# Kernel optimization log

Hardware: AMD Instinct MI355X
Metric: run time of the kernel (lower is better)

## Reference

```python
import jax, jax.numpy as jnp
import numpy as np

MAX_SPAN = 16
EPS = 1e-12


def setup_inputs() -> dict:
    key = jax.random.key(0)
    ks = jax.random.split(key, 10)
    B, S, H, R = 64, 512, 768, 51
    embed = jax.random.normal(ks[0], (B, S, H), dtype=jnp.float32)
    sub_head = jax.random.randint(ks[1], (B,), 0, S - MAX_SPAN, dtype=jnp.int32)
    span = jax.random.randint(ks[2], (B,), 0, MAX_SPAN, dtype=jnp.int32)
    sub_tail = sub_head + span  # guaranteed valid span inside [0, S)
    s = 0.02
    W_ih = jax.random.normal(ks[3], (4 * H, H), dtype=jnp.float32) * s
    W_hh = jax.random.normal(ks[4], (4 * H, H), dtype=jnp.float32) * s
    b_ih = jnp.zeros((4 * H,), dtype=jnp.float32)
    b_hh = jnp.zeros((4 * H,), dtype=jnp.float32)
    cln_weight = jnp.ones((H,), dtype=jnp.float32)
    cln_bias = jnp.zeros((H,), dtype=jnp.float32)
    # nonzero so the conditional path is exercised (init is zeros in torch)
    cln_Ww = jax.random.normal(ks[5], (H, H), dtype=jnp.float32) * s
    cln_Wb = jax.random.normal(ks[6], (H, H), dtype=jnp.float32) * s
    Wh = jax.random.normal(ks[7], (R, H), dtype=jnp.float32) * s
    bh = jnp.zeros((R,), dtype=jnp.float32)
    Wt = jax.random.normal(ks[8], (R, H), dtype=jnp.float32) * s
    bt = jnp.zeros((R,), dtype=jnp.float32)
    return {"embed": embed, "sub_head": sub_head, "sub_tail": sub_tail,
            "W_ih": W_ih, "W_hh": W_hh, "b_ih": b_ih, "b_hh": b_hh,
            "cln_weight": cln_weight, "cln_bias": cln_bias,
            "cln_Ww": cln_Ww, "cln_Wb": cln_Wb,
            "Wh": Wh, "bh": bh, "Wt": Wt, "bt": bt}


def _ragged_lstm(embed, sub_head, sub_tail, W_ih, W_hh, b_ih, b_hh):
    # Pack ragged spans [head, tail] into a padded [B, MAX_SPAN, H] block and
    # run one batched LSTM scan, freezing state once past each span's end.
    B, S, H = embed.shape
    offs = jnp.arange(MAX_SPAN, dtype=sub_head.dtype)
    pos = sub_head[:, None] + offs[None, :]                    # [B, T]
    idx = jnp.clip(pos, 0, S - 1)
    x = jnp.take_along_axis(embed, idx[:, :, None], axis=1)    # [B, T, H]
    mask = pos <= sub_tail[:, None]                            # [B, T]

    def step(carry, inp):
        h, c = carry
        xt, mt = inp                                           # [B,H], [B]
        gates = xt @ W_ih.T + b_ih + h @ W_hh.T + b_hh         # [B, 4H]
        i, f, g, o = jnp.split(gates, 4, axis=-1)
        c_new = jax.nn.sigmoid(f) * c + jax.nn.sigmoid(i) * jnp.tanh(g)
        h_new = jax.nn.sigmoid(o) * jnp.tanh(c_new)
        m = mt[:, None]
        h = jnp.where(m, h_new, h)
        c = jnp.where(m, c_new, c)
        return (h, c), None

    h0 = jnp.zeros((B, H), dtype=embed.dtype)
    (hn, _), _ = jax.lax.scan(step, (h0, h0),
                              (x.transpose(1, 0, 2), mask.T))
    return hn                                                  # [B, H]


def _cond_layernorm(inputs, cond, weight, bias, Ww, Wb):
    # weight/bias are conditioned on `cond` via zero-init dense layers
    w = cond @ Ww.T + weight                                   # [B, H]
    b = cond @ Wb.T + bias
    mu = jnp.mean(inputs, axis=-1, keepdims=True)
    xc = inputs - mu
    var = jnp.mean(xc * xc, axis=-1, keepdims=True)
    std = jnp.sqrt(var + EPS)
    return w[:, None, :] * xc / (std + EPS) + b[:, None, :]


def reference(embed, sub_head, sub_tail, W_ih, W_hh, b_ih, b_hh,
              cln_weight, cln_bias, cln_Ww, cln_Wb, Wh, bh, Wt, bt):
    sub_embed = _ragged_lstm(embed, sub_head, sub_tail, W_ih, W_hh, b_ih, b_hh)
    new_embed = _cond_layernorm(embed, sub_embed, cln_weight, cln_bias,
                                cln_Ww, cln_Wb)
    heads = jax.nn.sigmoid(new_embed @ Wh.T + bh)              # [B, S, R]
    tails = jax.nn.sigmoid(new_embed @ Wt.T + bt)
    return heads, tails
```

## Files before the change

### kernel.cpp

```cpp
#include <hip/hip_runtime.h>

typedef __attribute__((ext_vector_type(8))) short bhalf8;
typedef __attribute__((ext_vector_type(4))) float floatx4;

__device__ unsigned short g_whh[3072*768];
__device__ unsigned short g_wih[3072*768];
__device__ unsigned short g_wcln[1536*768];
__device__ unsigned short g_whl[128*768];
__device__ unsigned short g_h2[2*64*768];
__device__ float g_cbuf[64*768];
__device__ float g_xg[16*64*3072];
__device__ float g_wv[64*768], g_bv[64*768];
__device__ float g_bias[3072];
__device__ float g_cw[768], g_cb[768];
__device__ float g_bh[64], g_bt[64];

static __device__ __forceinline__ unsigned short f2bf(float f){
  unsigned u = __builtin_bit_cast(unsigned, f);
  u = (u + 0x7FFFu + ((u >> 16) & 1u)) >> 16;
  return (unsigned short)u;
}
static __device__ __forceinline__ float sigm(float x){ return 1.0f/(1.0f + __expf(-x)); }
static __device__ __forceinline__ float tanhq(float x){ float e = __expf(-2.0f*x); return (1.0f - e)/(1.0f + e); }

static __device__ __forceinline__ void cv8(const float* __restrict__ s, unsigned short* __restrict__ d){
  float4 a = ((const float4*)s)[0];
  float4 b = ((const float4*)s)[1];
  uint4 v;
  v.x = (unsigned)f2bf(a.x) | ((unsigned)f2bf(a.y) << 16);
  v.y = (unsigned)f2bf(a.z) | ((unsigned)f2bf(a.w) << 16);
  v.z = (unsigned)f2bf(b.x) | ((unsigned)f2bf(b.y) << 16);
  v.w = (unsigned)f2bf(b.z) | ((unsigned)f2bf(b.w) << 16);
  *(uint4*)d = v;
}

__global__ __launch_bounds__(256) void casrel_prep(
    const float* __restrict__ W_ih, const float* __restrict__ W_hh,
    const float* __restrict__ Ww,   const float* __restrict__ Wb,
    const float* __restrict__ Wh,   const float* __restrict__ Wt,
    const float* __restrict__ b_ih, const float* __restrict__ b_hh,
    const float* __restrict__ cw,   const float* __restrict__ cb,
    const float* __restrict__ bh,   const float* __restrict__ bt){
  const long CW = 294912;
  const long CC = 147456;
  const long CL = 12288;
  const long CH = 12288;
  const long CF = 6144;
  const long CB = 384, CV = 96, CR = 8;
  const long total = CW*2 + CC + CL + CH + CF + CB + CV*2 + CR*2;
  for(long i = (long)blockIdx.x*256 + threadIdx.x; i < total; i += (long)gridDim.x*256){
    long j = i;
    if(j < CW){ cv8(W_hh + j*8, g_whh + j*8); continue; } j -= CW;
    if(j < CW){ cv8(W_ih + j*8, g_wih + j*8); continue; } j -= CW;
    if(j < CC){ long e = j*8;
                if(e < 589824) cv8(Ww + e, g_wcln + e);
                else           cv8(Wb + (e - 589824), g_wcln + e);
                continue; } j -= CC;
    if(j < CL){ long e = j*8;
                long r = e / 768, k = e - r*768;
                if(r < 51)       cv8(Wh + r*768 + k, g_whl + e);
                else if(r < 102) cv8(Wt + (r-51)*768 + k, g_whl + e);
                else             *(uint4*)(g_whl + e) = make_uint4(0,0,0,0);
                continue; } j -= CL;
    if(j < CH){ *(uint4*)(g_h2 + j*8) = make_uint4(0,0,0,0); continue; } j -= CH;
    if(j < CF){ long e = j*8;
                *(float4*)(g_cbuf + e)     = make_float4(0,0,0,0);
                *(float4*)(g_cbuf + e + 4) = make_float4(0,0,0,0);
                continue; } j -= CF;
    if(j < CB){ long e = j*8;
                #pragma unroll
                for(int q=0;q<8;q++) g_bias[e+q] = b_ih[e+q] + b_hh[e+q];
                continue; } j -= CB;
    if(j < CV){ long e = j*8;
                *(float4*)(g_cw + e)     = *(const float4*)(cw + e);
                *(float4*)(g_cw + e + 4) = *(const float4*)(cw + e + 4);
                continue; } j -= CV;
    if(j < CV){ long e = j*8;
                *(float4*)(g_cb + e)     = *(const float4*)(cb + e);
                *(float4*)(g_cb + e + 4) = *(const float4*)(cb + e + 4);
                continue; } j -= CV;
    if(j < CR){ long e = j*8;
                #pragma unroll
                for(int q=0;q<8;q++){ long n = e+q; g_bh[n] = (n < 51) ? bh[n] : 0.0f; }
                continue; } j -= CR;
    { long e = j*8;
      #pragma unroll
      for(int q=0;q<8;q++){ long n = e+q; g_bt[n] = (n < 51) ? bt[n] : 0.0f; } }
  }
}

__global__ __launch_bounds__(256) void casrel_xgates(
    const float* __restrict__ embed, const int* __restrict__ head){
  __shared__ char sB[128*128];
  const int tid = threadIdx.x, l = tid & 63, w = tid >> 6;
  const int n0 = blockIdx.x * 128;
  const int m0 = blockIdx.y * 64 + w*16;
  const int mrow = m0 + (l & 15);
  const int b = mrow >> 4, t = mrow & 15;
  int pos = head[b] + t; pos = pos < 0 ? 0 : (pos > 511 ? 511 : pos);
  const float* aptr = embed + ((long)b*512 + pos)*768 + ((l >> 4)*8);
  floatx4 acc[8];
  #pragma unroll
  for(int q=0;q<8;q++){ acc[q][0]=0.f; acc[q][1]=0.f; acc[q][2]=0.f; acc[q][3]=0.f; }
  for(int kt=0; kt<12; ++kt){
    __syncthreads();
    #pragma unroll
    for(int j=0;j<4;j++){
      int f = tid + 256*j;
      int row = f >> 3, seg = f & 7;
      uint4 v = *(const uint4*)(g_wih + ((long)(n0+row))*768 + kt*64 + seg*8);
      *(uint4*)(sB + row*128 + ((seg*16) ^ ((row & 7) << 4))) = v;
    }
    __syncthreads();
    #pragma unroll
    for(int ks=0; ks<2; ++ks){
      const int k = kt*64 + ks*32;
      float4 lo = *(const float4*)(aptr + k);
      float4 hi = *(const float4*)(aptr + k + 4);
      bhalf8 a;
      a[0]=(short)f2bf(lo.x); a[1]=(short)f2bf(lo.y); a[2]=(short)f2bf(lo.z); a[3]=(short)f2bf(lo.w);
      a[4]=(short)f2bf(hi.x); a[5]=(short)f2bf(hi.y); a[6]=(short)f2bf(hi.z); a[7]=(short)f2bf(hi.w);
      const int kb = ks*64 + ((l >> 4)*16);
      #pragma unroll
      for(int q=0;q<8;q++){
        int row = q*16 + (l & 15);
        bhalf8 bb = *(const bhalf8*)(sB + row*128 + (kb ^ ((row & 7) << 4)));
        acc[q] = __builtin_amdgcn_mfma_f32_16x16x32_bf16(a, bb, acc[q], 0, 0, 0);
      }
    }
  }
  #pragma unroll
  for(int q=0;q<8;q++){
    const int n = n0 + q*16 + (l & 15);
    const float bias = g_bias[n];
    #pragma unroll
    for(int r=0;r<4;r++){
      const int m = m0 + (l >> 4)*4 + r;
      const int bb2 = m >> 4, tt = m & 15;
      g_xg[((long)(tt*64 + bb2))*3072 + n] = acc[q][r] + bias;
    }
  }
}

__global__ __launch_bounds__(256) void casrel_step(
    const int* __restrict__ head, const int* __restrict__ tail, int t){
  __shared__ char sW[32*1536];
  const unsigned short* hin = g_h2 + (t & 1)*49152;
  unsigned short* hout = g_h2 + ((t & 1) ^ 1)*49152;
  const int tid = threadIdx.x, l = tid & 63, w = tid >> 6;
  const int j0 = blockIdx.x * 8;
  #pragma unroll
  for(int j=0;j<12;j++){
    int f = tid + 256*j;
    int row = f / 96, seg = f - row*96;
    int grow = (row >> 3)*768 + j0 + (row & 7);
    uint4 v = *(const uint4*)(g_whh + (long)grow*768 + seg*8);
    *(uint4*)(sW + row*1536 + ((seg*16) ^ ((row & 7) << 4))) = v;
  }
  __syncthreads();
  const int arow = w*16 + (l & 15);
  floatx4 acc[2];
  #pragma unroll
  for(int q=0;q<2;q++){ acc[q][0]=0.f; acc[q][1]=0.f; acc[q][2]=0.f; acc[q][3]=0.f; }
  const unsigned short* ap = hin + arow*768 + ((l >> 4)*8);
  #pragma unroll 6
  for(int ks=0; ks<24; ++ks){
    bhalf8 a = *(const bhalf8*)(ap + ks*32);
    const int kb = ks*64 + ((l >> 4)*16);
    #pragma unroll
    for(int q=0;q<2;q++){
      int row = q*16 + (l & 15);
      bhalf8 bb = *(const bhalf8*)(sW + row*1536 + (kb ^ ((row & 7) << 4)));
      acc[q] = __builtin_amdgcn_mfma_f32_16x16x32_bf16(a, bb, acc[q], 0, 0, 0);
    }
  }
  const int c = l & 7;
  const int jown = j0 + c;
  const bool lo = (l & 8) == 0;
  #pragma unroll
  for(int r=0;r<4;r++){
    const int b = w*16 + (l >> 4)*4 + r;
    float v0 = acc[0][r], v1 = acc[1][r];
    float o0 = __shfl_xor(v0, 8);
    float o1 = __shfl_xor(v1, 8);
    if(lo){
      const int cell = b*768 + jown;
      const float* xp = g_xg + ((long)(t*64 + b))*3072 + jown;
      float Gi = v0 + xp[0];
      float Gf = o0 + xp[768];
      float Gg = v1 + xp[1536];
      float Go = o1 + xp[2304];
      if(t <= tail[b] - head[b]){
        float cc = g_cbuf[cell];
        float ig = sigm(Gi), fg = sigm(Gf), gg = tanhq(Gg), og = sigm(Go);
        cc = fg*cc + ig*gg;
        g_cbuf[cell] = cc;
        hout[cell] = f2bf(og*tanhq(cc));
      } else {
        hout[cell] = hin[cell];
      }
    }
  }
}

__global__ __launch_bounds__(256) void casrel_clnproj(){
  __shared__ char sW[32*1536];
  const int tid = threadIdx.x, l = tid & 63, w = tid >> 6;
  const int n0c = blockIdx.x * 32;
  #pragma unroll
  for(int j=0;j<12;j++){
    int f = tid + 256*j;
    int row = f / 96, seg = f - row*96;
    uint4 v = *(const uint4*)(g_wcln + (long)(n0c+row)*768 + seg*8);
    *(uint4*)(sW + row*1536 + ((seg*16) ^ ((row & 7) << 4))) = v;
  }
  __syncthreads();
  const int arow = w*16 + (l & 15);
  floatx4 acc2[2];
  #pragma unroll
  for(int q=0;q<2;q++){ acc2[q][0]=0.f; acc2[q][1]=0.f; acc2[q][2]=0.f; acc2[q][3]=0.f; }
  const unsigned short* ap2 = g_h2 + arow*768 + ((l >> 4)*8);
  for(int ks=0; ks<24; ++ks){
    bhalf8 a = *(const bhalf8*)(ap2 + ks*32);
    const int kb = ks*64 + ((l >> 4)*16);
    #pragma unroll
    for(int q=0;q<2;q++){
      int row = q*16 + (l & 15);
      bhalf8 bb = *(const bhalf8*)(sW + row*1536 + (kb ^ ((row & 7) << 4)));
      acc2[q] = __builtin_amdgcn_mfma_f32_16x16x32_bf16(a, bb, acc2[q], 0, 0, 0);
    }
  }
  #pragma unroll
  for(int q=0;q<2;q++){
    const int n = n0c + q*16 + (l & 15);
    #pragma unroll
    for(int r=0;r<4;r++){
      const int b = w*16 + (l >> 4)*4 + r;
      float v = acc2[q][r];
      if(n < 768) g_wv[b*768 + n] = v + g_cw[n];
      else        g_bv[b*768 + (n - 768)] = v + g_cb[n - 768];
    }
  }
}

__global__ __launch_bounds__(256) void casrel_out(
    const float* __restrict__ embed, float* __restrict__ out){
  __shared__ char sB[128*128];
  __shared__ char sE[32*128];
  __shared__ float sMu[32], sRs[32];
  const int tid = threadIdx.x, l = tid & 63, w = tid >> 6;
  const int b = blockIdx.y;
  const int s0 = blockIdx.x * 32;
  const float* xbase = embed + ((long)b*512 + s0)*768;
  for(int rr=0; rr<8; ++rr){
    const int row = w*8 + rr;
    const float* rp = xbase + row*768;
    float sm = 0.f, sq = 0.f;
    #pragma unroll
    for(int q=0;q<3;q++){
      float4 v = *(const float4*)(rp + l*4 + q*256);
      sm += v.x + v.y + v.z + v.w;
      sq += v.x*v.x + v.y*v.y + v.z*v.z + v.w*v.w;
    }
    #pragma unroll
    for(int o=32;o>0;o>>=1){ sm += __shfl_xor(sm, o); sq += __shfl_xor(sq, o); }
    if(l == 0){
      float mu = sm * (1.0f/768.0f);
      float var = sq * (1.0f/768.0f) - mu*mu;
      sMu[row] = mu;
      sRs[row] = 1.0f/(sqrtf(var + 1e-12f) + 1e-12f);
    }
  }
  __syncthreads();
  const int mf = w >> 1, nb = (w & 1)*4;
  floatx4 acc[4];
  #pragma unroll
  for(int q=0;q<4;q++){ acc[q][0]=0.f; acc[q][1]=0.f; acc[q][2]=0.f; acc[q][3]=0.f; }
  for(int kt=0; kt<12; ++kt){
    __syncthreads();
    #pragma unroll
    for(int j=0;j<4;j++){
      int f = tid + 256*j;
      int row = f >> 3, seg = f & 7;
      uint4 v = *(const uint4*)(g_whl + (long)row*768 + kt*64 + seg*8);
      *(uint4*)(sB + row*128 + ((seg*16) ^ ((row & 7) << 4))) = v;
    }
    #pragma unroll
    for(int j=0;j<2;j++){
      int f = tid + 256*j;
      int row = f >> 4, cs = f & 15;
      int k = kt*64 + cs*4;
      float4 x4 = *(const float4*)(xbase + row*768 + k);
      float4 w4 = *(const float4*)(g_wv + b*768 + k);
      float4 c4 = *(const float4*)(g_bv + b*768 + k);
      float mu = sMu[row], rs = sRs[row];
      unsigned long long pk =
          (unsigned long long)f2bf((x4.x - mu)*rs*w4.x + c4.x)
        | ((unsigned long long)f2bf((x4.y - mu)*rs*w4.y + c4.y) << 16)
        | ((unsigned long long)f2bf((x4.z - mu)*rs*w4.z + c4.z) << 32)
        | ((unsigned long long)f2bf((x4.w - mu)*rs*w4.w + c4.w) << 48);
      *(unsigned long long*)(sE + row*128 + ((cs*8) ^ ((row & 7) << 4))) = pk;
    }
    __syncthreads();
    #pragma unroll
    for(int ks=0; ks<2; ++ks){
      const int arow = mf*16 + (l & 15);
      const int kb = ks*64 + ((l >> 4)*16);
      bhalf8 a = *(const bhalf8*)(sE + arow*128 + (kb ^ ((arow & 7) << 4)));
      #pragma unroll
      for(int q=0;q<4;q++){
        int row = (nb + q)*16 + (l & 15);
        bhalf8 bb = *(const bhalf8*)(sB + row*128 + (kb ^ ((row & 7) << 4)));
        acc[q] = __builtin_amdgcn_mfma_f32_16x16x32_bf16(a, bb, acc[q], 0, 0, 0);
      }
    }
  }
  const long HT = (long)64*512*51;
  #pragma unroll
  for(int q=0;q<4;q++){
    const int n = (nb + q)*16 + (l & 15);
    if(n >= 102) continue;
    const int rr = (n < 51) ? n : (n - 51);
    const long obase = (n < 51) ? 0 : HT;
    const float bias = (n < 51) ? g_bh[n] : g_bt[n - 51];
    #pragma unroll
    for(int r=0;r<4;r++){
      const int s = s0 + mf*16 + (l >> 4)*4 + r;
      out[obase + ((long)b*512 + s)*51 + rr] = sigm(acc[q][r] + bias);
    }
  }
}

extern "C" void kernel_launch(void* const* d_in, const int* in_sizes, int n_in,
                              void* d_out, int out_size, void* d_ws, size_t ws_size,
                              hipStream_t stream){
  const float* embed = (const float*)d_in[0];
  const int*   head  = (const int*)d_in[1];
  const int*   tail  = (const int*)d_in[2];
  const float* W_ih  = (const float*)d_in[3];
  const float* W_hh  = (const float*)d_in[4];
  const float* b_ih  = (const float*)d_in[5];
  const float* b_hh  = (const float*)d_in[6];
  const float* cw    = (const float*)d_in[7];
  const float* cb    = (const float*)d_in[8];
  const float* Ww    = (const float*)d_in[9];
  const float* Wb    = (const float*)d_in[10];
  const float* Wh    = (const float*)d_in[11];
  const float* bh    = (const float*)d_in[12];
  const float* Wt    = (const float*)d_in[13];
  const float* bt    = (const float*)d_in[14];
  float* out = (float*)d_out;
  (void)d_ws; (void)ws_size;

  casrel_prep<<<dim3(2048), dim3(256), 0, stream>>>(W_ih, W_hh, Ww, Wb, Wh, Wt,
                                                    b_ih, b_hh, cw, cb, bh, bt);
  casrel_xgates<<<dim3(24,16), dim3(256), 0, stream>>>(embed, head);
  for(int t=0; t<16; ++t)
    casrel_step<<<dim3(96), dim3(256), 0, stream>>>(head, tail, t);
  casrel_clnproj<<<dim3(48), dim3(256), 0, stream>>>();
  casrel_out<<<dim3(16,64), dim3(256), 0, stream>>>(embed, out);
}
```

Before: 245.3 us.

## Convert weights to bf16 on the fly in consumers and store gate preactivations as bf16

Stops pre-converting W_ih and the CLN weights in the prep kernel. The xgates and clnproj kernels now read the fp32 weights and pack them to bf16 while loading tiles. The x-gate buffer is stored as bf16 instead of fp32, halving its write and read traffic. The output kernel double-buffers the normalized-activation tile and reads the projection weights straight from global memory instead of staging them in shared memory. This removes a full weight conversion pass and some barriers, at the cost of extra rounding of the gate preactivations and uncached global B loads.

Result: slower. 276.9 us (+12.9%).

```diff
diff --git a/kernel.cpp b/kernel.cpp
--- a/kernel.cpp
+++ b/kernel.cpp
@@ -4,12 +4,10 @@
 typedef __attribute__((ext_vector_type(4))) float floatx4;
 
 __device__ unsigned short g_whh[3072*768];
-__device__ unsigned short g_wih[3072*768];
-__device__ unsigned short g_wcln[1536*768];
 __device__ unsigned short g_whl[128*768];
 __device__ unsigned short g_h2[2*64*768];
 __device__ float g_cbuf[64*768];
-__device__ float g_xg[16*64*3072];
+__device__ unsigned short g_xg[16*64*3072];
 __device__ float g_wv[64*768], g_bv[64*768];
 __device__ float g_bias[3072];
 __device__ float g_cw[768], g_cb[768];
@@ -20,10 +18,14 @@
   u = (u + 0x7FFFu + ((u >> 16) & 1u)) >> 16;
   return (unsigned short)u;
 }
+static __device__ __forceinline__ float bf2f(unsigned short v){
+  unsigned u = ((unsigned)v) << 16;
+  return __builtin_bit_cast(float, u);
+}
 static __device__ __forceinline__ float sigm(float x){ return 1.0f/(1.0f + __expf(-x)); }
 static __device__ __forceinline__ float tanhq(float x){ float e = __expf(-2.0f*x); return (1.0f - e)/(1.0f + e); }
 
-static __device__ __forceinline__ void cv8(const float* __restrict__ s, unsigned short* __restrict__ d){
+static __device__ __forceinline__ uint4 pk8(const float* __restrict__ s){
   float4 a = ((const float4*)s)[0];
   float4 b = ((const float4*)s)[1];
   uint4 v;
@@ -31,35 +33,28 @@
   v.y = (unsigned)f2bf(a.z) | ((unsigned)f2bf(a.w) << 16);
   v.z = (unsigned)f2bf(b.x) | ((unsigned)f2bf(b.y) << 16);
   v.w = (unsigned)f2bf(b.z) | ((unsigned)f2bf(b.w) << 16);
-  *(uint4*)d = v;
+  return v;
 }
 
 __global__ __launch_bounds__(256) void casrel_prep(
-    const float* __restrict__ W_ih, const float* __restrict__ W_hh,
-    const float* __restrict__ Ww,   const float* __restrict__ Wb,
+    const float* __restrict__ W_hh,
     const float* __restrict__ Wh,   const float* __restrict__ Wt,
     const float* __restrict__ b_ih, const float* __restrict__ b_hh,
     const float* __restrict__ cw,   const float* __restrict__ cb,
     const float* __restrict__ bh,   const float* __restrict__ bt){
   const long CW = 294912;
-  const long CC = 147456;
   const long CL = 12288;
   const long CH = 12288;
   const long CF = 6144;
   const long CB = 384, CV = 96, CR = 8;
-  const long total = CW*2 + CC + CL + CH + CF + CB + CV*2 + CR*2;
+  const long total = CW + CL + CH + CF + CB + CV*2 + CR*2;
   for(long i = (long)blockIdx.x*256 + threadIdx.x; i < total; i += (long)gridDim.x*256){
     long j = i;
-    if(j < CW){ cv8(W_hh + j*8, g_whh + j*8); continue; } j -= CW;
-    if(j < CW){ cv8(W_ih + j*8, g_wih + j*8); continue; } j -= CW;
-    if(j < CC){ long e = j*8;
-                if(e < 589824) cv8(Ww + e, g_wcln + e);
-                else           cv8(Wb + (e - 589824), g_wcln + e);
-                continue; } j -= CC;
+    if(j < CW){ *(uint4*)(g_whh + j*8) = pk8(W_hh + j*8); continue; } j -= CW;
     if(j < CL){ long e = j*8;
                 long r = e / 768, k = e - r*768;
-                if(r < 51)       cv8(Wh + r*768 + k, g_whl + e);
-                else if(r < 102) cv8(Wt + (r-51)*768 + k, g_whl + e);
+                if(r < 51)       *(uint4*)(g_whl + e) = pk8(Wh + r*768 + k);
+                else if(r < 102) *(uint4*)(g_whl + e) = pk8(Wt + (r-51)*768 + k);
                 else             *(uint4*)(g_whl + e) = make_uint4(0,0,0,0);
                 continue; } j -= CL;
     if(j < CH){ *(uint4*)(g_h2 + j*8) = make_uint4(0,0,0,0); continue; } j -= CH;
@@ -90,7 +85,8 @@
 }
 
 __global__ __launch_bounds__(256) void casrel_xgates(
-    const float* __restrict__ embed, const int* __restrict__ head){
+    const float* __restrict__ embed, const int* __restrict__ head,
+    const float* __restrict__ W_ih){
   __shared__ char sB[128*128];
   const int tid = threadIdx.x, l = tid & 63, w = tid >> 6;
   const int n0 = blockIdx.x * 128;
@@ -108,7 +104,7 @@
     for(int j=0;j<4;j++){
       int f = tid + 256*j;
       int row = f >> 3, seg = f & 7;
-      uint4 v = *(const uint4*)(g_wih + ((long)(n0+row))*768 + kt*64 + seg*8);
+      uint4 v = pk8(W_ih + ((long)(n0+row))*768 + kt*64 + seg*8);
       *(uint4*)(sB + row*128 + ((seg*16) ^ ((row & 7) << 4))) = v;
     }
     __syncthreads();
@@ -137,7 +133,7 @@
     for(int r=0;r<4;r++){
       const int m = m0 + (l >> 4)*4 + r;
       const int bb2 = m >> 4, tt = m & 15;
-      g_xg[((long)(tt*64 + bb2))*3072 + n] = acc[q][r] + bias;
+      g_xg[((long)(tt*64 + bb2))*3072 + n] = f2bf(acc[q][r] + bias);
     }
   }
 }
@@ -185,11 +181,11 @@
     float o1 = __shfl_xor(v1, 8);
     if(lo){
       const int cell = b*768 + jown;
-      const float* xp = g_xg + ((long)(t*64 + b))*3072 + jown;
-      float Gi = v0 + xp[0];
-      float Gf = o0 + xp[768];
-      float Gg = v1 + xp[1536];
-      float Go = o1 + xp[2304];
+      const unsigned short* xp = g_xg + ((long)(t*64 + b))*3072 + jown;
+      float Gi = v0 + bf2f(xp[0]);
+      float Gf = o0 + bf2f(xp[768]);
+      float Gg = v1 + bf2f(xp[1536]);
+      float Go = o1 + bf2f(xp[2304]);
       if(t <= tail[b] - head[b]){
         float cc = g_cbuf[cell];
         float ig = sigm(Gi), fg = sigm(Gf), gg = tanhq(Gg), og = sigm(Go);
@@ -203,7 +199,8 @@
   }
 }
 
-__global__ __launch_bounds__(256) void casrel_clnproj(){
+__global__ __launch_bounds__(256) void casrel_clnproj(
+    const float* __restrict__ Ww, const float* __restrict__ Wb){
   __shared__ char sW[32*1536];
   const int tid = threadIdx.x, l = tid & 63, w = tid >> 6;
   const int n0c = blockIdx.x * 32;
@@ -211,7 +208,9 @@
   for(int j=0;j<12;j++){
     int f = tid + 256*j;
     int row = f / 96, seg = f - row*96;
-    uint4 v = *(const uint4*)(g_wcln + (long)(n0c+row)*768 + seg*8);
+    const int n = n0c + row;
+    uint4 v = (n < 768) ? pk8(Ww + (long)n*768 + seg*8)
+                        : pk8(Wb + (long)(n-768)*768 + seg*8);
     *(uint4*)(sW + row*1536 + ((seg*16) ^ ((row & 7) << 4))) = v;
   }
   __syncthreads();
@@ -245,8 +244,7 @@
 
 __global__ __launch_bounds__(256) void casrel_out(
     const float* __restrict__ embed, float* __restrict__ out){
-  __shared__ char sB[128*128];
-  __shared__ char sE[32*128];
+  __shared__ char sE[2][32*128];
   __shared__ float sMu[32], sRs[32];
   const int tid = threadIdx.x, l = tid & 63, w = tid >> 6;
   const int b = blockIdx.y;
@@ -277,14 +275,7 @@
   #pragma unroll
   for(int q=0;q<4;q++){ acc[q][0]=0.f; acc[q][1]=0.f; acc[q][2]=0.f; acc[q][3]=0.f; }
   for(int kt=0; kt<12; ++kt){
-    __syncthreads();
-    #pragma unroll
-    for(int j=0;j<4;j++){
-      int f = tid + 256*j;
-      int row = f >> 3, seg = f & 7;
-      uint4 v = *(const uint4*)(g_whl + (long)row*768 + kt*64 + seg*8);
-      *(uint4*)(sB + row*128 + ((seg*16) ^ ((row & 7) << 4))) = v;
-    }
+    char* se = sE[kt & 1];
     #pragma unroll
     for(int j=0;j<2;j++){
       int f = tid + 256*j;
@@ -299,18 +290,19 @@
         | ((unsigned long long)f2bf((x4.y - mu)*rs*w4.y + c4.y) << 16)
         | ((unsigned long long)f2bf((x4.z - mu)*rs*w4.z + c4.z) << 32)
         | ((unsigned long long)f2bf((x4.w - mu)*rs*w4.w + c4.w) << 48);
-      *(unsigned long long*)(sE + row*128 + ((cs*8) ^ ((row & 7) << 4))) = pk;
+      *(unsigned long long*)(se + row*128 + ((cs*8) ^ ((row & 7) << 4))) = pk;
     }
     __syncthreads();
     #pragma unroll
     for(int ks=0; ks<2; ++ks){
       const int arow = mf*16 + (l & 15);
       const int kb = ks*64 + ((l >> 4)*16);
-      bhalf8 a = *(const bhalf8*)(sE + arow*128 + (kb ^ ((arow & 7) << 4)));
+      bhalf8 a = *(const bhalf8*)(se + arow*128 + (kb ^ ((arow & 7) << 4)));
+      const int kcol = kt*64 + ks*32 + ((l >> 4)*8);
       #pragma unroll
       for(int q=0;q<4;q++){
         int row = (nb + q)*16 + (l & 15);
-        bhalf8 bb = *(const bhalf8*)(sB + row*128 + (kb ^ ((row & 7) << 4)));
+        bhalf8 bb = *(const bhalf8*)(g_whl + (long)row*768 + kcol);
         acc[q] = __builtin_amdgcn_mfma_f32_16x16x32_bf16(a, bb, acc[q], 0, 0, 0);
       }
     }
@@ -352,11 +344,10 @@
   float* out = (float*)d_out;
   (void)d_ws; (void)ws_size;
 
-  casrel_prep<<<dim3(2048), dim3(256), 0, stream>>>(W_ih, W_hh, Ww, Wb, Wh, Wt,
-                                                    b_ih, b_hh, cw, cb, bh, bt);
-  casrel_xgates<<<dim3(24,16), dim3(256), 0, stream>>>(embed, head);
+  casrel_prep<<<dim3(1024), dim3(256), 0, stream>>>(W_hh, Wh, Wt, b_ih, b_hh, cw, cb, bh, bt);
+  casrel_xgates<<<dim3(24,16), dim3(256), 0, stream>>>(embed, head, W_ih);
   for(int t=0; t<16; ++t)
     casrel_step<<<dim3(96), dim3(256), 0, stream>>>(head, tail, t);
-  casrel_clnproj<<<dim3(48), dim3(256), 0, stream>>>();
+  casrel_clnproj<<<dim3(48), dim3(256), 0, stream>>>(Ww, Wb);
   casrel_out<<<dim3(16,64), dim3(256), 0, stream>>>(embed, out);
 }
```
